# Optimization experiments

Measured on AMD Instinct MI355X. Metric: run time of the kernel, lower is better.

The kernel has to match this reference:

```python
import jax, jax.numpy as jnp
import numpy as np

N, E, G, H = 4096, 8192, 64, 128  # nodes, edges, graphs, hidden dim
NODE_DIM, EDGE_DIM = 11, 5


def _linear_params(key, fan_in, fan_out):
    kw, kb = jax.random.split(key)
    s = 1.0 / np.sqrt(fan_in)
    w = jax.random.uniform(kw, (fan_in, fan_out), minval=-s, maxval=s, dtype=jnp.float32)
    b = jax.random.uniform(kb, (fan_out,), minval=-s, maxval=s, dtype=jnp.float32)
    return w, b


def setup_inputs() -> dict:
    key = jax.random.key(0)
    ks = jax.random.split(key, 10)
    x = jax.random.normal(ks[0], (N, NODE_DIM), dtype=jnp.float32)
    edge_attr = jax.random.normal(ks[1], (E, EDGE_DIM), dtype=jnp.float32)
    edge_index = jax.random.randint(ks[2], (2, E), 0, N, dtype=jnp.int64)
    batch = jnp.sort(jax.random.randint(ks[3], (N,), 0, G, dtype=jnp.int64))
    # preprocess MLP: node_dim -> 128 -> 128
    p1_w, p1_b = _linear_params(ks[4], NODE_DIM, H)
    p2_w, p2_b = _linear_params(ks[5], H, H)
    # edge net: edge_dim -> 128 -> 256 -> 128 -> 128*128 (ReLU between, none after last)
    e1_w, e1_b = _linear_params(ks[6], EDGE_DIM, 128)
    e2_w, e2_b = _linear_params(ks[7], 128, 256)
    e3_w, e3_b = _linear_params(ks[8], 256, 128)
    e4_w, e4_b = _linear_params(ks[9], 128, H * H)
    return {"x": x, "edge_attr": edge_attr, "edge_index": edge_index, "batch": batch,
            "p1_w": p1_w, "p1_b": p1_b, "p2_w": p2_w, "p2_b": p2_b,
            "e1_w": e1_w, "e1_b": e1_b, "e2_w": e2_w, "e2_b": e2_b,
            "e3_w": e3_w, "e3_b": e3_b, "e4_w": e4_w, "e4_b": e4_b}


def reference(x, edge_attr, edge_index, batch,
              p1_w, p1_b, p2_w, p2_b,
              e1_w, e1_b, e2_w, e2_b, e3_w, e3_b, e4_w, e4_b):
    # node preprocess MLP (maps 11-dim features to 128 so NNConv dims are consistent)
    h = jax.nn.relu(x @ p1_w + p1_b) @ p2_w + p2_b  # [N, H]
    # edge network -> per-edge weight matrix [E, H, H]
    e = jax.nn.relu(edge_attr @ e1_w + e1_b)
    e = jax.nn.relu(e @ e2_w + e2_b)
    e = jax.nn.relu(e @ e3_w + e3_b)
    W = (e @ e4_w + e4_b).reshape(E, H, H)
    # NNConv (root_weight=False, bias=False, aggr='mean'):
    src, dst = edge_index[0], edge_index[1]
    msg = jnp.einsum('ei,eio->eo', h[src], W)  # gather + per-edge matmul, [E, H]
    agg = jax.ops.segment_sum(msg, dst, num_segments=N)
    cnt = jax.ops.segment_sum(jnp.ones((E,), msg.dtype), dst, num_segments=N)
    h_out = agg / jnp.maximum(cnt, 1.0)[:, None]  # scatter-mean, [N, H]
    # global add pool over graphs
    pooled = jax.ops.segment_sum(h_out, batch, num_segments=G)  # [G, H]
    return pooled
```

## Files before the change

### kernel.cpp

```cpp
#include <hip/hip_runtime.h>
#include <hip/hip_bf16.h>

#define N_NODES 4096
#define N_EDGES 8192
#define N_GRAPHS 64
#define HDIM 128

typedef __attribute__((ext_vector_type(8))) short bf16x8;
typedef __attribute__((ext_vector_type(4))) float f32x4;
typedef __attribute__((ext_vector_type(4))) unsigned short u16x4;

static __device__ __forceinline__ unsigned short f2bf(float f) {
    unsigned u = __builtin_bit_cast(unsigned, f);
    u += 0x7fffu + ((u >> 16) & 1u);
    return (unsigned short)(u >> 16);
}
static __device__ __forceinline__ float bf2f(unsigned short s) {
    unsigned u = ((unsigned)s) << 16;
    return __builtin_bit_cast(float, u);
}

__global__ __launch_bounds__(256) void fused_pre_kernel(
    const float* __restrict__ x, const float* __restrict__ p1w, const float* __restrict__ p1b,
    const float* __restrict__ p2w, const float* __restrict__ p2b, const float* __restrict__ e4b,
    unsigned short* __restrict__ h_bf, float* __restrict__ hb,
    const float* __restrict__ ea, const float* __restrict__ w1, const float* __restrict__ b1,
    const float* __restrict__ w2, const float* __restrict__ b2,
    const float* __restrict__ w3, const float* __restrict__ b3,
    unsigned short* __restrict__ e3bf,
    const float* __restrict__ w4, unsigned short* __restrict__ w4perm)
{
    __shared__ __align__(16) char smem[33024];
    const int t = threadIdx.x;
    const int bid = blockIdx.x;

    if (bid < 512) {
        float (*es)[5]   = (float(*)[5])smem;
        float (*l1t)[16] = (float(*)[16])(smem + 320);
        float (*l2t)[16] = (float(*)[16])(smem + 8512);
        const int eb = bid * 16;

        for (int r = t; r < 80; r += 256) es[r / 5][r % 5] = ea[(eb + r / 5) * 5 + r % 5];
        __syncthreads();
        {
            int j = t & 127;
            float wd[5];
            #pragma unroll
            for (int d = 0; d < 5; ++d) wd[d] = w1[d * 128 + j];
            float bj = b1[j];
            for (int p = 0; p < 8; ++p) {
                int e = p * 2 + (t >> 7);
                float acc = bj;
                #pragma unroll
                for (int d = 0; d < 5; ++d) acc += es[e][d] * wd[d];
                l1t[j][e] = fmaxf(acc, 0.f);
            }
        }
        __syncthreads();
        {
            float acc[16];
            float bj = b2[t];
            #pragma unroll
            for (int r = 0; r < 16; ++r) acc[r] = bj;
            for (int k = 0; k < 128; ++k) {
                float w = w2[k * 256 + t];
                const float4* row = (const float4*)&l1t[k][0];
                float4 v0 = row[0], v1 = row[1], v2 = row[2], v3 = row[3];
                acc[0]  += v0.x * w; acc[1]  += v0.y * w; acc[2]  += v0.z * w; acc[3]  += v0.w * w;
                acc[4]  += v1.x * w; acc[5]  += v1.y * w; acc[6]  += v1.z * w; acc[7]  += v1.w * w;
                acc[8]  += v2.x * w; acc[9]  += v2.y * w; acc[10] += v2.z * w; acc[11] += v2.w * w;
                acc[12] += v3.x * w; acc[13] += v3.y * w; acc[14] += v3.z * w; acc[15] += v3.w * w;
            }
            #pragma unroll
            for (int r = 0; r < 16; ++r) l2t[t][r] = fmaxf(acc[r], 0.f);
        }
        __syncthreads();
        {
            int j = t & 127, eh = t >> 7;
            float acc[8];
            float bj = b3[j];
            #pragma unroll
            for (int r = 0; r < 8; ++r) acc[r] = bj;
            for (int k = 0; k < 256; ++k) {
                float w = w3[k * 128 + j];
                const float4* row = (const float4*)&l2t[k][eh * 8];
                float4 v0 = row[0], v1 = row[1];
                acc[0] += v0.x * w; acc[1] += v0.y * w; acc[2] += v0.z * w; acc[3] += v0.w * w;
                acc[4] += v1.x * w; acc[5] += v1.y * w; acc[6] += v1.z * w; acc[7] += v1.w * w;
            }
            #pragma unroll
            for (int r = 0; r < 8; ++r)
                e3bf[(eb + eh * 8 + r) * 128 + j] = f2bf(fmaxf(acc[r], 0.f));
        }
    } else if (bid < 768) {
        float (*xs)[11]  = (float(*)[11])smem;
        float (*l1t)[16] = (float(*)[16])(smem + 704);
        float (*hs)[16]  = (float(*)[16])(smem + 8896);
        const int nb = bid - 512;

        for (int r = t; r < 16 * 11; r += 256) {
            int e = r / 11, d = r % 11;
            xs[e][d] = x[(nb * 16 + e) * 11 + d];
        }
        __syncthreads();
        {
            int j = t & 127;
            float wd[11];
            #pragma unroll
            for (int d = 0; d < 11; ++d) wd[d] = p1w[d * 128 + j];
            float bj = p1b[j];
            for (int p = 0; p < 8; ++p) {
                int e = p * 2 + (t >> 7);
                float acc = bj;
                #pragma unroll
                for (int d = 0; d < 11; ++d) acc += xs[e][d] * wd[d];
                l1t[j][e] = fmaxf(acc, 0.f);
            }
        }
        __syncthreads();
        {
            int j = t & 127, eh = t >> 7;
            float acc[8];
            float bj = p2b[j];
            #pragma unroll
            for (int r = 0; r < 8; ++r) acc[r] = bj;
            for (int k = 0; k < 128; ++k) {
                float w = p2w[k * 128 + j];
                const float4* row = (const float4*)&l1t[k][eh * 8];
                float4 v0 = row[0], v1 = row[1];
                acc[0] += v0.x * w; acc[1] += v0.y * w; acc[2] += v0.z * w; acc[3] += v0.w * w;
                acc[4] += v1.x * w; acc[5] += v1.y * w; acc[6] += v1.z * w; acc[7] += v1.w * w;
            }
            #pragma unroll
            for (int r = 0; r < 8; ++r) {
                int e = eh * 8 + r;
                h_bf[(nb * 16 + e) * 128 + j] = f2bf(acc[r]);
                hs[j][e] = acc[r];
            }
        }
        __syncthreads();
        {
            int j = t & 127, eh = t >> 7;
            float acc[8] = {0.f,0.f,0.f,0.f,0.f,0.f,0.f,0.f};
            for (int i = 0; i < 128; ++i) {
                float w = e4b[i * 128 + j];
                const float4* row = (const float4*)&hs[i][eh * 8];
                float4 v0 = row[0], v1 = row[1];
                acc[0] += v0.x * w; acc[1] += v0.y * w; acc[2] += v0.z * w; acc[3] += v0.w * w;
                acc[4] += v1.x * w; acc[5] += v1.y * w; acc[6] += v1.z * w; acc[7] += v1.w * w;
            }
            #pragma unroll
            for (int r = 0; r < 8; ++r) hb[(nb * 16 + eh * 8 + r) * 128 + j] = acc[r];
        }
    } else {
        unsigned short (*tt)[129] = (unsigned short(*)[129])smem;
        const int i = bid - 768;
        for (int r = t; r < 16384; r += 256) {
            int k = r >> 7, o = r & 127;
            tt[o][k] = f2bf(w4[k * 16384 + i * 128 + o]);
        }
        __syncthreads();
        for (int r = t; r < 16384; r += 256) {
            int o = r >> 7, k = r & 127;
            w4perm[((size_t)(o >> 5) * 128 + i) * 4352 + (size_t)(o & 31) * 136 + k] = tt[o][k];
        }
    }
}

__global__ __launch_bounds__(256, 3) void nnconv_kernel(
    const unsigned short* __restrict__ e3bf, const unsigned short* __restrict__ h_bf,
    const unsigned short* __restrict__ w4perm, const float* __restrict__ hb,
    const int* __restrict__ ei, float* __restrict__ agg, float* __restrict__ cnt)
{
    __shared__ __align__(16) float ht_f[64 * 128];
    const int t = threadIdx.x;
    const int bid = blockIdx.x;
    const int xcd    = bid & 7;
    const int osplit = xcd >> 1;
    const int ksplit = xcd & 1;
    const int etile  = bid >> 3;
    const int w = t >> 6, lane = t & 63, q = lane >> 4, l15 = lane & 15;
    const int mg = w >> 1;
    const int og = w & 1;
    const int e0 = etile * 128;
    const int o0 = osplit * 32;
    const int i0 = ksplit * 64;

    bf16x8 afrag[4][4];
    #pragma unroll
    for (int mb = 0; mb < 4; ++mb)
        #pragma unroll
        for (int s = 0; s < 4; ++s) {
            int row = e0 + mg * 64 + mb * 16 + l15;
            afrag[mb][s] = *(const bf16x8*)(e3bf + row * 128 + s * 32 + q * 8);
        }

    {
        int r = t >> 1, part = t & 1;
        int s = ei[e0 + r];
        #pragma unroll
        for (int u = 0; u < 4; ++u) {
            uint4 v = *(const uint4*)(h_bf + (size_t)s * 128 + i0 + part * 32 + u * 8);
            const unsigned short* pv = (const unsigned short*)&v;
            #pragma unroll
            for (int j = 0; j < 8; ++j)
                ht_f[(part * 32 + u * 8 + j) * 128 + r] = bf2f(pv[j]);
        }
    }

    f32x4 acc[4];
    #pragma unroll
    for (int mb = 0; mb < 4; ++mb) acc[mb] = (f32x4){0.f, 0.f, 0.f, 0.f};
    const f32x4 zero4 = (f32x4){0.f, 0.f, 0.f, 0.f};

    __syncthreads();

    const unsigned short* bbase =
        w4perm + (size_t)(osplit * 128 + i0) * 4352 + (og * 16 + l15) * 136 + q * 8;
    #pragma unroll 2
    for (int c = 0; c < 64; ++c) {
        const unsigned short* bp = bbase + (size_t)c * 4352;
        bf16x8 bfrag[4];
        #pragma unroll
        for (int s = 0; s < 4; ++s)
            bfrag[s] = *(const bf16x8*)(bp + s * 32);
        #pragma unroll
        for (int mb = 0; mb < 4; ++mb) {
            f32x4 hv = *(const f32x4*)&ht_f[c * 128 + mg * 64 + mb * 16 + q * 4];
            f32x4 tmp = __builtin_amdgcn_mfma_f32_16x16x32_bf16(afrag[mb][0], bfrag[0], zero4, 0, 0, 0);
            tmp = __builtin_amdgcn_mfma_f32_16x16x32_bf16(afrag[mb][1], bfrag[1], tmp, 0, 0, 0);
            tmp = __builtin_amdgcn_mfma_f32_16x16x32_bf16(afrag[mb][2], bfrag[2], tmp, 0, 0, 0);
            tmp = __builtin_amdgcn_mfma_f32_16x16x32_bf16(afrag[mb][3], bfrag[3], tmp, 0, 0, 0);
            #pragma unroll
            for (int r = 0; r < 4; ++r)
                acc[mb][r] += hv[r] * tmp[r];
        }
    }

    #pragma unroll
    for (int mb = 0; mb < 4; ++mb) {
        #pragma unroll
        for (int r = 0; r < 4; ++r) {
            int e = e0 + mg * 64 + mb * 16 + q * 4 + r;
            int de = ei[N_EDGES + e];
            int se = ei[e];
            if (xcd == 0 && og == 0 && l15 == 0) atomicAdd(&cnt[de], 1.0f);
            int o = o0 + og * 16 + l15;
            float v = acc[mb][r];
            if (ksplit == 0) v += hb[(size_t)se * 128 + o];
            atomicAdd(&agg[(size_t)de * 128 + o], v);
        }
    }
}

__global__ __launch_bounds__(128) void pool_kernel(
    const float* __restrict__ agg, const float* __restrict__ cnt,
    const int* __restrict__ batch, float* __restrict__ out)
{
    const int g = blockIdx.x, t = threadIdx.x;
    int lo = 0, hi = N_NODES;
    while (lo < hi) { int m = (lo + hi) >> 1; if (batch[m] < g) lo = m + 1; else hi = m; }
    const int n_lo = lo;
    int lo2 = n_lo, hi2 = N_NODES;
    while (lo2 < hi2) { int m = (lo2 + hi2) >> 1; if (batch[m] < g + 1) lo2 = m + 1; else hi2 = m; }
    const int n_hi = lo2;

    float s0 = 0.f, s1 = 0.f, s2 = 0.f, s3 = 0.f;
    int n = n_lo;
    for (; n + 4 <= n_hi; n += 4) {
        float c0 = cnt[n], c1 = cnt[n + 1], c2 = cnt[n + 2], c3 = cnt[n + 3];
        float v0 = agg[(n    ) * 128 + t];
        float v1 = agg[(n + 1) * 128 + t];
        float v2 = agg[(n + 2) * 128 + t];
        float v3 = agg[(n + 3) * 128 + t];
        s0 += v0 / (c0 > 1.f ? c0 : 1.f);
        s1 += v1 / (c1 > 1.f ? c1 : 1.f);
        s2 += v2 / (c2 > 1.f ? c2 : 1.f);
        s3 += v3 / (c3 > 1.f ? c3 : 1.f);
    }
    for (; n < n_hi; ++n) {
        float c = cnt[n];
        s0 += agg[n * 128 + t] / (c > 1.f ? c : 1.f);
    }
    out[g * 128 + t] = (s0 + s1) + (s2 + s3);
}

extern "C" void kernel_launch(void* const* d_in, const int* in_sizes, int n_in,
                              void* d_out, int out_size, void* d_ws, size_t ws_size,
                              hipStream_t stream)
{
    const float* x     = (const float*)d_in[0];
    const float* ea    = (const float*)d_in[1];
    const int*   ei    = (const int*)d_in[2];
    const int*   batch = (const int*)d_in[3];
    const float* p1w   = (const float*)d_in[4];
    const float* p1b   = (const float*)d_in[5];
    const float* p2w   = (const float*)d_in[6];
    const float* p2b   = (const float*)d_in[7];
    const float* w1    = (const float*)d_in[8];
    const float* b1    = (const float*)d_in[9];
    const float* w2    = (const float*)d_in[10];
    const float* b2    = (const float*)d_in[11];
    const float* w3    = (const float*)d_in[12];
    const float* b3    = (const float*)d_in[13];
    const float* w4    = (const float*)d_in[14];
    const float* b4    = (const float*)d_in[15];
    float* out = (float*)d_out;
    (void)in_sizes; (void)n_in; (void)out_size; (void)ws_size;

    char* ws = (char*)d_ws;
    unsigned short* h_bf = (unsigned short*)(ws);
    unsigned short* e3bf = (unsigned short*)(ws + 1048576);
    float* hb            = (float*)(ws + 3145728);
    unsigned short* w4p  = (unsigned short*)(ws + 5242880);
    float* agg           = (float*)(ws + 9699328);
    float* cnt           = (float*)(ws + 11796480);

    hipMemsetAsync(agg, 0, (size_t)N_NODES * 128 * 4 + (size_t)N_NODES * 4, stream);

    fused_pre_kernel<<<896, 256, 0, stream>>>(
        x, p1w, p1b, p2w, p2b, b4, h_bf, hb,
        ea, w1, b1, w2, b2, w3, b3, e3bf,
        w4, w4p);
    nnconv_kernel<<<512, 256, 0, stream>>>(e3bf, h_bf, w4p, hb, ei, agg, cnt);
    pool_kernel<<<N_GRAPHS, 128, 0, stream>>>(agg, cnt, batch, out);
}
```

Measured before the change: 183.9 us.

## Move edge MLP layers 2-3 to a bf16 MFMA kernel and retile NNConv

Layers 2 and 3 of the edge network move out of the fused preprocess kernel, which ran them as scalar fp32 loops, into a new kernel that uses bf16 MFMA. The preprocess kernel now also converts w2 and w3 into padded bf16 layouts and writes the layer-1 output as bf16, reusing the agg buffer region before it is zeroed. NNConv now splits outputs 8 ways with 16 columns each, launches twice as many blocks with smaller per-wave tiles, and raises occupancy. The changes add a kernel launch and lower the edge MLP to bf16 precision.

```diff
diff --git a/kernel.cpp b/kernel.cpp
--- a/kernel.cpp
+++ b/kernel.cpp
@@ -8,7 +8,6 @@
 
 typedef __attribute__((ext_vector_type(8))) short bf16x8;
 typedef __attribute__((ext_vector_type(4))) float f32x4;
-typedef __attribute__((ext_vector_type(4))) unsigned short u16x4;
 
 static __device__ __forceinline__ unsigned short f2bf(float f) {
     unsigned u = __builtin_bit_cast(unsigned, f);
@@ -20,83 +19,25 @@
     return __builtin_bit_cast(float, u);
 }
 
-__global__ __launch_bounds__(256) void fused_pre_kernel(
+__global__ __launch_bounds__(256) void pre_kernel(
     const float* __restrict__ x, const float* __restrict__ p1w, const float* __restrict__ p1b,
     const float* __restrict__ p2w, const float* __restrict__ p2b, const float* __restrict__ e4b,
     unsigned short* __restrict__ h_bf, float* __restrict__ hb,
     const float* __restrict__ ea, const float* __restrict__ w1, const float* __restrict__ b1,
-    const float* __restrict__ w2, const float* __restrict__ b2,
-    const float* __restrict__ w3, const float* __restrict__ b3,
-    unsigned short* __restrict__ e3bf,
-    const float* __restrict__ w4, unsigned short* __restrict__ w4perm)
+    const float* __restrict__ w4, unsigned short* __restrict__ w4perm,
+    const float* __restrict__ w2, unsigned short* __restrict__ w2p,
+    const float* __restrict__ w3, unsigned short* __restrict__ w3p,
+    unsigned short* __restrict__ l1bf)
 {
     __shared__ __align__(16) char smem[33024];
     const int t = threadIdx.x;
     const int bid = blockIdx.x;
 
-    if (bid < 512) {
-        float (*es)[5]   = (float(*)[5])smem;
-        float (*l1t)[16] = (float(*)[16])(smem + 320);
-        float (*l2t)[16] = (float(*)[16])(smem + 8512);
-        const int eb = bid * 16;
-
-        for (int r = t; r < 80; r += 256) es[r / 5][r % 5] = ea[(eb + r / 5) * 5 + r % 5];
-        __syncthreads();
-        {
-            int j = t & 127;
-            float wd[5];
-            #pragma unroll
-            for (int d = 0; d < 5; ++d) wd[d] = w1[d * 128 + j];
-            float bj = b1[j];
-            for (int p = 0; p < 8; ++p) {
-                int e = p * 2 + (t >> 7);
-                float acc = bj;
-                #pragma unroll
-                for (int d = 0; d < 5; ++d) acc += es[e][d] * wd[d];
-                l1t[j][e] = fmaxf(acc, 0.f);
-            }
-        }
-        __syncthreads();
-        {
-            float acc[16];
-            float bj = b2[t];
-            #pragma unroll
-            for (int r = 0; r < 16; ++r) acc[r] = bj;
-            for (int k = 0; k < 128; ++k) {
-                float w = w2[k * 256 + t];
-                const float4* row = (const float4*)&l1t[k][0];
-                float4 v0 = row[0], v1 = row[1], v2 = row[2], v3 = row[3];
-                acc[0]  += v0.x * w; acc[1]  += v0.y * w; acc[2]  += v0.z * w; acc[3]  += v0.w * w;
-                acc[4]  += v1.x * w; acc[5]  += v1.y * w; acc[6]  += v1.z * w; acc[7]  += v1.w * w;
-                acc[8]  += v2.x * w; acc[9]  += v2.y * w; acc[10] += v2.z * w; acc[11] += v2.w * w;
-                acc[12] += v3.x * w; acc[13] += v3.y * w; acc[14] += v3.z * w; acc[15] += v3.w * w;
-            }
-            #pragma unroll
-            for (int r = 0; r < 16; ++r) l2t[t][r] = fmaxf(acc[r], 0.f);
-        }
-        __syncthreads();
-        {
-            int j = t & 127, eh = t >> 7;
-            float acc[8];
-            float bj = b3[j];
-            #pragma unroll
-            for (int r = 0; r < 8; ++r) acc[r] = bj;
-            for (int k = 0; k < 256; ++k) {
-                float w = w3[k * 128 + j];
-                const float4* row = (const float4*)&l2t[k][eh * 8];
-                float4 v0 = row[0], v1 = row[1];
-                acc[0] += v0.x * w; acc[1] += v0.y * w; acc[2] += v0.z * w; acc[3] += v0.w * w;
-                acc[4] += v1.x * w; acc[5] += v1.y * w; acc[6] += v1.z * w; acc[7] += v1.w * w;
-            }
-            #pragma unroll
-            for (int r = 0; r < 8; ++r)
-                e3bf[(eb + eh * 8 + r) * 128 + j] = f2bf(fmaxf(acc[r], 0.f));
-        }
-    } else if (bid < 768) {
+    if (bid < 256) {
         float (*xs)[11]  = (float(*)[11])smem;
         float (*l1t)[16] = (float(*)[16])(smem + 704);
         float (*hs)[16]  = (float(*)[16])(smem + 8896);
-        const int nb = bid - 512;
+        const int nb = bid;
 
         for (int r = t; r < 16 * 11; r += 256) {
             int e = r / 11, d = r % 11;
@@ -152,9 +93,9 @@
             #pragma unroll
             for (int r = 0; r < 8; ++r) hb[(nb * 16 + eh * 8 + r) * 128 + j] = acc[r];
         }
-    } else {
+    } else if (bid < 384) {
         unsigned short (*tt)[129] = (unsigned short(*)[129])smem;
-        const int i = bid - 768;
+        const int i = bid - 256;
         for (int r = t; r < 16384; r += 256) {
             int k = r >> 7, o = r & 127;
             tt[o][k] = f2bf(w4[k * 16384 + i * 128 + o]);
@@ -164,10 +105,138 @@
             int o = r >> 7, k = r & 127;
             w4perm[((size_t)(o >> 5) * 128 + i) * 4352 + (size_t)(o & 31) * 136 + k] = tt[o][k];
         }
-    }
-}
-
-__global__ __launch_bounds__(256, 3) void nnconv_kernel(
+    } else if (bid < 386) {
+        unsigned short (*tt)[129] = (unsigned short(*)[129])smem;
+        const int oh = bid - 384;
+        for (int r = t; r < 16384; r += 256) {
+            int k = r >> 7, ol = r & 127;
+            tt[ol][k] = f2bf(w2[k * 256 + oh * 128 + ol]);
+        }
+        __syncthreads();
+        for (int r = t; r < 16384; r += 256) {
+            int ol = r >> 7, k = r & 127;
+            w2p[(oh * 128 + ol) * 136 + k] = tt[ol][k];
+        }
+    } else if (bid < 388) {
+        unsigned short (*tt)[257] = (unsigned short(*)[257])smem;
+        const int oh = bid - 386;
+        for (int r = t; r < 16384; r += 256) {
+            int k = r >> 6, ol = r & 63;
+            tt[ol][k] = f2bf(w3[k * 128 + oh * 64 + ol]);
+        }
+        __syncthreads();
+        for (int r = t; r < 16384; r += 256) {
+            int ol = r >> 8, k = r & 255;
+            w3p[(oh * 64 + ol) * 264 + k] = tt[ol][k];
+        }
+    } else {
+        float (*es)[5] = (float(*)[5])smem;
+        const int eb = (bid - 388) * 256;
+        for (int r = t; r < 1280; r += 256) ((float*)es)[r] = ea[eb * 5 + r];
+        __syncthreads();
+        int j = t & 127, eh = t >> 7;
+        float wd[5];
+        #pragma unroll
+        for (int d = 0; d < 5; ++d) wd[d] = w1[d * 128 + j];
+        float bj = b1[j];
+        for (int p = 0; p < 128; ++p) {
+            int e = eh * 128 + p;
+            float acc = bj;
+            #pragma unroll
+            for (int d = 0; d < 5; ++d) acc += es[e][d] * wd[d];
+            l1bf[(size_t)(eb + e) * 128 + j] = f2bf(fmaxf(acc, 0.f));
+        }
+    }
+}
+
+__global__ __launch_bounds__(256, 2) void edge23_kernel(
+    const unsigned short* __restrict__ l1bf,
+    const float* __restrict__ b2, const float* __restrict__ b3,
+    const unsigned short* __restrict__ w2p, const unsigned short* __restrict__ w3p,
+    unsigned short* __restrict__ e3bf)
+{
+    __shared__ __align__(16) unsigned short l2a[32 * 264];
+    const int t = threadIdx.x, bid = blockIdx.x;
+    const int w = t >> 6, lane = t & 63, q = lane >> 4, l15 = lane & 15;
+    const int e0 = bid * 32;
+    const f32x4 zero4 = (f32x4){0.f, 0.f, 0.f, 0.f};
+
+    bf16x8 afrag[2][4];
+    #pragma unroll
+    for (int mb = 0; mb < 2; ++mb)
+        #pragma unroll
+        for (int s = 0; s < 4; ++s)
+            afrag[mb][s] = *(const bf16x8*)(l1bf + (size_t)(e0 + mb * 16 + l15) * 128 + s * 32 + q * 8);
+
+    f32x4 acc[2][4];
+    #pragma unroll
+    for (int mb = 0; mb < 2; ++mb)
+        #pragma unroll
+        for (int ob = 0; ob < 4; ++ob) acc[mb][ob] = zero4;
+    #pragma unroll
+    for (int ob = 0; ob < 4; ++ob) {
+        const int o = w * 64 + ob * 16 + l15;
+        bf16x8 bfrag[4];
+        #pragma unroll
+        for (int s = 0; s < 4; ++s)
+            bfrag[s] = *(const bf16x8*)(w2p + (size_t)o * 136 + s * 32 + q * 8);
+        #pragma unroll
+        for (int mb = 0; mb < 2; ++mb) {
+            f32x4 tmp = __builtin_amdgcn_mfma_f32_16x16x32_bf16(afrag[mb][0], bfrag[0], zero4, 0, 0, 0);
+            tmp = __builtin_amdgcn_mfma_f32_16x16x32_bf16(afrag[mb][1], bfrag[1], tmp, 0, 0, 0);
+            tmp = __builtin_amdgcn_mfma_f32_16x16x32_bf16(afrag[mb][2], bfrag[2], tmp, 0, 0, 0);
+            acc[mb][ob] = __builtin_amdgcn_mfma_f32_16x16x32_bf16(afrag[mb][3], bfrag[3], tmp, 0, 0, 0);
+        }
+    }
+    #pragma unroll
+    for (int mb = 0; mb < 2; ++mb)
+        #pragma unroll
+        for (int ob = 0; ob < 4; ++ob) {
+            int o = w * 64 + ob * 16 + l15;
+            float bo = b2[o];
+            #pragma unroll
+            for (int r = 0; r < 4; ++r) {
+                int e_loc = mb * 16 + q * 4 + r;
+                l2a[e_loc * 264 + o] = f2bf(fmaxf(acc[mb][ob][r] + bo, 0.f));
+            }
+        }
+    __syncthreads();
+
+    f32x4 acc3[2][2];
+    #pragma unroll
+    for (int mb = 0; mb < 2; ++mb)
+        #pragma unroll
+        for (int ob = 0; ob < 2; ++ob) acc3[mb][ob] = zero4;
+    #pragma unroll
+    for (int ks = 0; ks < 8; ++ks) {
+        bf16x8 a3[2];
+        #pragma unroll
+        for (int mb = 0; mb < 2; ++mb)
+            a3[mb] = *(const bf16x8*)&l2a[(mb * 16 + l15) * 264 + ks * 32 + q * 8];
+        #pragma unroll
+        for (int ob = 0; ob < 2; ++ob) {
+            const int o = w * 32 + ob * 16 + l15;
+            bf16x8 bf = *(const bf16x8*)(w3p + (size_t)o * 264 + ks * 32 + q * 8);
+            #pragma unroll
+            for (int mb = 0; mb < 2; ++mb)
+                acc3[mb][ob] = __builtin_amdgcn_mfma_f32_16x16x32_bf16(a3[mb], bf, acc3[mb][ob], 0, 0, 0);
+        }
+    }
+    #pragma unroll
+    for (int mb = 0; mb < 2; ++mb)
+        #pragma unroll
+        for (int ob = 0; ob < 2; ++ob) {
+            int o = w * 32 + ob * 16 + l15;
+            float bo = b3[o];
+            #pragma unroll
+            for (int r = 0; r < 4; ++r) {
+                int e = e0 + mb * 16 + q * 4 + r;
+                e3bf[(size_t)e * 128 + o] = f2bf(fmaxf(acc3[mb][ob][r] + bo, 0.f));
+            }
+        }
+}
+
+__global__ __launch_bounds__(256, 4) void nnconv_kernel(
     const unsigned short* __restrict__ e3bf, const unsigned short* __restrict__ h_bf,
     const unsigned short* __restrict__ w4perm, const float* __restrict__ hb,
     const int* __restrict__ ei, float* __restrict__ agg, float* __restrict__ cnt)
@@ -175,24 +244,21 @@
     __shared__ __align__(16) float ht_f[64 * 128];
     const int t = threadIdx.x;
     const int bid = blockIdx.x;
-    const int xcd    = bid & 7;
-    const int osplit = xcd >> 1;
-    const int ksplit = xcd & 1;
-    const int etile  = bid >> 3;
+    const int osplit = bid & 7;
+    const int ksplit = (bid >> 3) & 1;
+    const int etile  = bid >> 4;
     const int w = t >> 6, lane = t & 63, q = lane >> 4, l15 = lane & 15;
-    const int mg = w >> 1;
-    const int og = w & 1;
     const int e0 = etile * 128;
-    const int o0 = osplit * 32;
+    const int o0 = osplit * 16;
     const int i0 = ksplit * 64;
 
-    bf16x8 afrag[4][4];
-    #pragma unroll
-    for (int mb = 0; mb < 4; ++mb)
+    bf16x8 afrag[2][4];
+    #pragma unroll
+    for (int mb = 0; mb < 2; ++mb)
         #pragma unroll
         for (int s = 0; s < 4; ++s) {
-            int row = e0 + mg * 64 + mb * 16 + l15;
-            afrag[mb][s] = *(const bf16x8*)(e3bf + row * 128 + s * 32 + q * 8);
+            int row = e0 + w * 32 + mb * 16 + l15;
+            afrag[mb][s] = *(const bf16x8*)(e3bf + (size_t)row * 128 + s * 32 + q * 8);
         }
 
     {
@@ -208,15 +274,16 @@
         }
     }
 
-    f32x4 acc[4];
-    #pragma unroll
-    for (int mb = 0; mb < 4; ++mb) acc[mb] = (f32x4){0.f, 0.f, 0.f, 0.f};
+    f32x4 acc[2];
+    acc[0] = (f32x4){0.f, 0.f, 0.f, 0.f};
+    acc[1] = (f32x4){0.f, 0.f, 0.f, 0.f};
     const f32x4 zero4 = (f32x4){0.f, 0.f, 0.f, 0.f};
 
     __syncthreads();
 
     const unsigned short* bbase =
-        w4perm + (size_t)(osplit * 128 + i0) * 4352 + (og * 16 + l15) * 136 + q * 8;
+        w4perm + ((size_t)(osplit >> 1) * 128 + i0) * 4352
+               + (size_t)((osplit & 1) * 16 + l15) * 136 + q * 8;
     #pragma unroll 2
     for (int c = 0; c < 64; ++c) {
         const unsigned short* bp = bbase + (size_t)c * 4352;
@@ -225,8 +292,8 @@
         for (int s = 0; s < 4; ++s)
             bfrag[s] = *(const bf16x8*)(bp + s * 32);
         #pragma unroll
-        for (int mb = 0; mb < 4; ++mb) {
-            f32x4 hv = *(const f32x4*)&ht_f[c * 128 + mg * 64 + mb * 16 + q * 4];
+        for (int mb = 0; mb < 2; ++mb) {
+            f32x4 hv = *(const f32x4*)&ht_f[c * 128 + w * 32 + mb * 16 + q * 4];
             f32x4 tmp = __builtin_amdgcn_mfma_f32_16x16x32_bf16(afrag[mb][0], bfrag[0], zero4, 0, 0, 0);
             tmp = __builtin_amdgcn_mfma_f32_16x16x32_bf16(afrag[mb][1], bfrag[1], tmp, 0, 0, 0);
             tmp = __builtin_amdgcn_mfma_f32_16x16x32_bf16(afrag[mb][2], bfrag[2], tmp, 0, 0, 0);
@@ -238,14 +305,14 @@
     }
 
     #pragma unroll
-    for (int mb = 0; mb < 4; ++mb) {
+    for (int mb = 0; mb < 2; ++mb) {
         #pragma unroll
         for (int r = 0; r < 4; ++r) {
-            int e = e0 + mg * 64 + mb * 16 + q * 4 + r;
+            int e = e0 + w * 32 + mb * 16 + q * 4 + r;
             int de = ei[N_EDGES + e];
             int se = ei[e];
-            if (xcd == 0 && og == 0 && l15 == 0) atomicAdd(&cnt[de], 1.0f);
-            int o = o0 + og * 16 + l15;
+            if (osplit == 0 && ksplit == 0 && l15 == 0) atomicAdd(&cnt[de], 1.0f);
+            int o = o0 + l15;
             float v = acc[mb][r];
             if (ksplit == 0) v += hb[(size_t)se * 128 + o];
             atomicAdd(&agg[(size_t)de * 128 + o], v);
@@ -314,14 +381,16 @@
     float* hb            = (float*)(ws + 3145728);
     unsigned short* w4p  = (unsigned short*)(ws + 5242880);
     float* agg           = (float*)(ws + 9699328);
+    unsigned short* l1bf = (unsigned short*)(ws + 9699328);
     float* cnt           = (float*)(ws + 11796480);
-
+    unsigned short* w2p  = (unsigned short*)(ws + 11812864);
+    unsigned short* w3p  = (unsigned short*)(ws + 11882496);
+
+    pre_kernel<<<420, 256, 0, stream>>>(
+        x, p1w, p1b, p2w, p2b, b4, h_bf, hb,
+        ea, w1, b1, w4, w4p, w2, w2p, w3, w3p, l1bf);
+    edge23_kernel<<<256, 256, 0, stream>>>(l1bf, b2, b3, w2p, w3p, e3bf);
     hipMemsetAsync(agg, 0, (size_t)N_NODES * 128 * 4 + (size_t)N_NODES * 4, stream);
-
-    fused_pre_kernel<<<896, 256, 0, stream>>>(
-        x, p1w, p1b, p2w, p2b, b4, h_bf, hb,
-        ea, w1, b1, w2, b2, w3, b3, e3bf,
-        w4, w4p);
-    nnconv_kernel<<<512, 256, 0, stream>>>(e3bf, h_bf, w4p, hb, ei, agg, cnt);
+    nnconv_kernel<<<1024, 256, 0, stream>>>(e3bf, h_bf, w4p, hb, ei, agg, cnt);
     pool_kernel<<<N_GRAPHS, 128, 0, stream>>>(agg, cnt, batch, out);
 }
```

Result: slower. 206.2 us (+12.1%).
